# Kernel tuning notes

Measured on AMD Instinct MI355X. Metric: run time of the kernel, lower is better.

## Reference

```python
import jax, jax.numpy as jnp
import numpy as np

D_K = 64
SCALE = 1.0 / (D_K ** 0.5)
NEG = -1.0e9

def setup_inputs() -> dict:
    key = jax.random.key(0)
    kq, kk, kv, km = jax.random.split(key, 4)
    B, H, S, D = 4, 16, 2048, D_K
    query = jax.random.normal(kq, (B, H, S, D), dtype=jnp.float32)
    k_ = jax.random.normal(kk, (B, H, S, D), dtype=jnp.float32)
    v_ = jax.random.normal(kv, (B, H, S, D), dtype=jnp.float32)
    mask = jax.random.randint(km, (B, 1, S, S), 0, 2, dtype=jnp.int32)
    return {"query": query, "key": k_, "value": v_, "mask": mask}

def reference(query, key, value, mask):
    # scores: [B, H, S, S]
    scores = jnp.einsum('bhqd,bhkd->bhqk', query, key) * SCALE
    scores = jnp.where(mask == 0, NEG, scores)
    attn = jax.nn.softmax(scores, axis=-1)
    return jnp.einsum('bhqk,bhkd->bhqd', attn, value)
```

## Files before the change

kernel.cpp:

```cpp
#include <hip/hip_runtime.h>

typedef _Float16 f16x8 __attribute__((ext_vector_type(8)));
typedef _Float16 f16x4 __attribute__((ext_vector_type(4)));
typedef _Float16 f16x2 __attribute__((ext_vector_type(2)));
typedef float    f32x4 __attribute__((ext_vector_type(4)));
typedef unsigned long long u64;

constexpr int Bc = 4, Hc = 16, Sc = 2048, Dc = 64;
constexpr int KVBLK = 64;
constexpr int NKV = Sc / KVBLK;
constexpr int QB  = 128;
constexpr int NQT = Sc / QB;
constexpr int NQ  = 32;

__device__ __forceinline__ float fast_exp2(float x) {
#if __has_builtin(__builtin_amdgcn_exp2f)
  return __builtin_amdgcn_exp2f(x);
#else
  return exp2f(x);
#endif
}

__device__ __forceinline__ void gload16(const void* g, void* l) {
  __builtin_amdgcn_global_load_lds(
      (const __attribute__((address_space(1))) void*)g,
      (__attribute__((address_space(3))) void*)l, 16, 0, 0);
}

__device__ __forceinline__ f32x4 mfma16(f16x8 a, f16x8 b, f32x4 c) {
  return __builtin_amdgcn_mfma_f32_16x16x32_f16(a, b, c, 0, 0, 0);
}

__device__ __forceinline__ float dot2acc(unsigned pk, float acc) {
#if __has_builtin(__builtin_amdgcn_fdot2)
  const f16x2 one2 = {(_Float16)1.f, (_Float16)1.f};
  return __builtin_amdgcn_fdot2(__builtin_bit_cast(f16x2, pk), one2, acc, false);
#else
  const f16x2 v = __builtin_bit_cast(f16x2, pk);
  return acc + (float)v[0] + (float)v[1];
#endif
}

__global__ __launch_bounds__(256)
void cvt_k_sw(const float* __restrict__ K, _Float16* __restrict__ Ko) {
  const int tile = blockIdx.x;
  const int t = threadIdx.x;
  const float* src = K + (size_t)tile * 4096;
  _Float16* dst = Ko + (size_t)tile * 4096;
  #pragma unroll
  for (int cc = 0; cc < 2; ++cc) {
    const int c = t + cc * 256;
    const int r = c >> 3, s = c & 7;
    const int ss = s ^ (r & 7);
    const float* p = src + r * 64 + ss * 8;
    const float4 a = *(const float4*)p;
    const float4 b2 = *(const float4*)(p + 4);
    f16x8 h = {(_Float16)a.x, (_Float16)a.y, (_Float16)a.z, (_Float16)a.w,
               (_Float16)b2.x, (_Float16)b2.y, (_Float16)b2.z, (_Float16)b2.w};
    *(f16x8*)(dst + (size_t)c * 8) = h;
  }
}

__global__ __launch_bounds__(256)
void cvt_v_sw(const float* __restrict__ V, _Float16* __restrict__ Vo) {
  __shared__ float tile[64][65];
  const int tb = blockIdx.x;
  const int t = threadIdx.x;
  const float* src = V + (size_t)tb * 4096;
  {
    const int r = t >> 2, c0 = (t & 3) * 16;
    #pragma unroll
    for (int j = 0; j < 16; j += 4)
      *(float4*)&tile[r][c0 + j] = *(const float4*)(src + r * 64 + c0 + j);
  }
  __syncthreads();
  _Float16* dst = Vo + (size_t)tb * 4096;
  #pragma unroll
  for (int cc = 0; cc < 2; ++cc) {
    const int c = t + cc * 256;
    const int d = c >> 3, ss = c & 7;
    const int m = ss ^ (d & 7);
    const int ks = m >> 2, lg = m & 3;
    f16x8 h;
    #pragma unroll
    for (int e = 0; e < 8; ++e) {
      const int key = 32 * ks + 16 * (e >> 2) + 4 * lg + (e & 3);
      h[e] = (_Float16)tile[key][d];
    }
    *(f16x8*)(dst + (size_t)c * 8) = h;
  }
}

__global__ __launch_bounds__(256)
void pack_mask(const int* __restrict__ M, u64* __restrict__ MB) {
  const int gid  = blockIdx.x * 256 + threadIdx.x;
  const int wv   = gid >> 6, lane = gid & 63;
  const int kv   = wv & (NKV - 1);
  const int row  = (wv >> 5) & (Sc - 1);
  const int b    = wv >> 16;
  const int m    = M[((size_t)b * Sc + row) * Sc + (size_t)kv * 64 + lane];
  const u64 bits = __ballot(m != 0);
  if (lane == 0)
    MB[(((size_t)b * NQ + (row >> 6)) * NKV + kv) * 64 + (row & 63)] = bits;
}

__global__ __launch_bounds__(256, 4)
void attn_fwd6(const float* __restrict__ Q, const _Float16* __restrict__ Ksw,
               const _Float16* __restrict__ Vsw, const u64* __restrict__ MB,
               float* __restrict__ O)
{
  const int bid = (blockIdx.x & 7) * 128 + (blockIdx.x >> 3);
  const int qt  = bid & (NQT - 1);
  const int bh  = bid >> 4;
  const int b   = bh >> 4;
  const int q0  = qt * QB;

  const int tid = threadIdx.x;
  const int w   = tid >> 6;
  const int l   = tid & 63;
  const int lg  = l >> 4;
  const int lc  = l & 15;

  __shared__ _Float16 Kbuf0[4096], Kbuf1[4096];
  __shared__ _Float16 Vbuf0[4096], Vbuf1[4096];

  f16x8 qf[2][2];
  {
    const float qs = 0.125f * 1.4426950408889634f;
    #pragma unroll
    for (int qa = 0; qa < 2; ++qa) {
      const float* qr = Q + ((size_t)bh * Sc + q0 + w * 32 + qa * 16 + lc) * Dc + 8 * lg;
      #pragma unroll
      for (int ks = 0; ks < 2; ++ks) {
        f16x8 t;
        #pragma unroll
        for (int e = 0; e < 8; ++e) t[e] = (_Float16)(qr[ks * 32 + e] * qs);
        qf[qa][ks] = t;
      }
    }
  }

  f32x4 o_acc[2][4];
  #pragma unroll
  for (int qa = 0; qa < 2; ++qa)
    #pragma unroll
    for (int nt = 0; nt < 4; ++nt) o_acc[qa][nt] = (f32x4){0.f, 0.f, 0.f, 0.f};
  float l_acc0 = 0.f, l_acc1 = 0.f;
  const float NEGL = -1.4426950e9f;

  const char* KswT = (const char*)(Ksw + (size_t)bh * Sc * Dc);
  const char* VswT = (const char*)(Vsw + (size_t)bh * Sc * Dc);
  const int row0 = q0 + w * 32 + lc;
  const int row1 = row0 + 16;
  const u64* Mb0 = MB + ((size_t)(b * NQ + (row0 >> 6)) * NKV) * 64 + (row0 & 63);
  const u64* Mb1 = MB + ((size_t)(b * NQ + (row1 >> 6)) * NKV) * 64 + (row1 & 63);

  const int sw0 = (lg * 16) ^ ((lc & 7) << 4);
  const int sw1 = (64 + lg * 16) ^ ((lc & 7) << 4);

  auto stage = [&](int kvt, _Float16* kb, _Float16* vb) {
    const char* g = (w < 2) ? KswT + (size_t)kvt * 8192 + w * 4096
                            : VswT + (size_t)kvt * 8192 + (w - 2) * 4096;
    char* lb = (w < 2) ? (char*)kb + w * 4096
                       : (char*)vb + (w - 2) * 4096;
    #pragma unroll
    for (int j = 0; j < 4; ++j)
      gload16(g + j * 1024 + l * 16, lb + j * 1024);
  };

  auto body = [&](const _Float16* kb, const _Float16* vb, u64 mb0, u64 mb1) {
    const char* Kb = (const char*)kb;
    f32x4 p[2][4];
    __builtin_amdgcn_s_setprio(1);
    #pragma unroll
    for (int nt = 0; nt < 4; ++nt) {
      const f16x8 k0 = *(const f16x8*)(Kb + (nt * 16 + lc) * 128 + sw0);
      const f16x8 k1 = *(const f16x8*)(Kb + (nt * 16 + lc) * 128 + sw1);
      #pragma unroll
      for (int qa = 0; qa < 2; ++qa) {
        f32x4 acc = (f32x4){0.f, 0.f, 0.f, 0.f};
        acc = mfma16(k0, qf[qa][0], acc);
        acc = mfma16(k1, qf[qa][1], acc);
        p[qa][nt] = acc;
      }
    }
    __builtin_amdgcn_s_setprio(0);

    #pragma unroll
    for (int qa = 0; qa < 2; ++qa) {
      const u64 mbits = qa ? mb1 : mb0;
      #pragma unroll
      for (int nt = 0; nt < 4; ++nt) {
        const unsigned b4 = ((unsigned)(mbits >> (nt * 16 + 4 * lg))) & 0xFu;
        #pragma unroll
        for (int r = 0; r < 4; ++r) {
          const float s = ((b4 >> r) & 1u) ? p[qa][nt][r] : NEGL;
          p[qa][nt][r] = fast_exp2(s);
        }
      }
    }

    f16x8 pa0[2], pa1[2];
    #pragma unroll
    for (int qa = 0; qa < 2; ++qa) {
      uint4 u0, u1;
      u0.x = __builtin_bit_cast(unsigned, __builtin_amdgcn_cvt_pkrtz(p[qa][0][0], p[qa][0][1]));
      u0.y = __builtin_bit_cast(unsigned, __builtin_amdgcn_cvt_pkrtz(p[qa][0][2], p[qa][0][3]));
      u0.z = __builtin_bit_cast(unsigned, __builtin_amdgcn_cvt_pkrtz(p[qa][1][0], p[qa][1][1]));
      u0.w = __builtin_bit_cast(unsigned, __builtin_amdgcn_cvt_pkrtz(p[qa][1][2], p[qa][1][3]));
      u1.x = __builtin_bit_cast(unsigned, __builtin_amdgcn_cvt_pkrtz(p[qa][2][0], p[qa][2][1]));
      u1.y = __builtin_bit_cast(unsigned, __builtin_amdgcn_cvt_pkrtz(p[qa][2][2], p[qa][2][3]));
      u1.z = __builtin_bit_cast(unsigned, __builtin_amdgcn_cvt_pkrtz(p[qa][3][0], p[qa][3][1]));
      u1.w = __builtin_bit_cast(unsigned, __builtin_amdgcn_cvt_pkrtz(p[qa][3][2], p[qa][3][3]));
      float la = qa ? l_acc1 : l_acc0;
      la = dot2acc(u0.x, la); la = dot2acc(u0.y, la);
      la = dot2acc(u0.z, la); la = dot2acc(u0.w, la);
      la = dot2acc(u1.x, la); la = dot2acc(u1.y, la);
      la = dot2acc(u1.z, la); la = dot2acc(u1.w, la);
      if (qa) l_acc1 = la; else l_acc0 = la;
      pa0[qa] = __builtin_bit_cast(f16x8, u0);
      pa1[qa] = __builtin_bit_cast(f16x8, u1);
    }

    const char* Vb = (const char*)vb;
    __builtin_amdgcn_s_setprio(1);
    #pragma unroll
    for (int nt = 0; nt < 4; ++nt) {
      const f16x8 v0 = *(const f16x8*)(Vb + (nt * 16 + lc) * 128 + sw0);
      const f16x8 v1 = *(const f16x8*)(Vb + (nt * 16 + lc) * 128 + sw1);
      o_acc[0][nt] = mfma16(pa0[0], v0, o_acc[0][nt]);
      o_acc[0][nt] = mfma16(pa1[0], v1, o_acc[0][nt]);
      o_acc[1][nt] = mfma16(pa0[1], v0, o_acc[1][nt]);
      o_acc[1][nt] = mfma16(pa1[1], v1, o_acc[1][nt]);
    }
    __builtin_amdgcn_s_setprio(0);
  };

  u64 n0 = Mb0[0], n1 = Mb1[0];
  stage(0, Kbuf0, Vbuf0);
  __syncthreads();
  for (int kv = 0; kv < NKV; kv += 2) {
    const u64 a0 = n0, a1 = n1;
    const u64 c0 = Mb0[(size_t)(kv + 1) * 64];
    const u64 c1 = Mb1[(size_t)(kv + 1) * 64];
    stage(kv + 1, Kbuf1, Vbuf1);
    body(Kbuf0, Vbuf0, a0, a1);
    __syncthreads();
    if (kv + 2 < NKV) {
      n0 = Mb0[(size_t)(kv + 2) * 64];
      n1 = Mb1[(size_t)(kv + 2) * 64];
      stage(kv + 2, Kbuf0, Vbuf0);
    }
    body(Kbuf1, Vbuf1, c0, c1);
    __syncthreads();
  }

  l_acc0 += __shfl_xor(l_acc0, 16, 64);
  l_acc0 += __shfl_xor(l_acc0, 32, 64);
  l_acc1 += __shfl_xor(l_acc1, 16, 64);
  l_acc1 += __shfl_xor(l_acc1, 32, 64);
  #pragma unroll
  for (int qa = 0; qa < 2; ++qa) {
    #pragma unroll
    for (int r = 0; r < 4; ++r) {
      const float li = 1.0f / __shfl(qa ? l_acc1 : l_acc0, 4 * lg + r, 64);
      float* orow = O + ((size_t)bh * Sc + q0 + w * 32 + qa * 16 + 4 * lg + r) * Dc + lc;
      #pragma unroll
      for (int nt = 0; nt < 4; ++nt)
        orow[nt * 16] = o_acc[qa][nt][r] * li;
    }
  }
}

constexpr int LDSW = KVBLK + 8;

__global__ __launch_bounds__(256)
void attn_fwd_v1(const float* __restrict__ Q, const float* __restrict__ K,
                 const float* __restrict__ V, const int* __restrict__ M,
                 float* __restrict__ O)
{
  const int bid   = blockIdx.x;
  const int qtile = bid & 31;
  const int bh    = bid >> 5;
  const int b     = bh >> 4;

  const float* Qp = Q + ((size_t)bh * Sc + (size_t)qtile * 64) * Dc;
  const float* Kp = K + (size_t)bh * Sc * Dc;
  const float* Vp = V + (size_t)bh * Sc * Dc;
  const int*   Mp = M + (size_t)b * Sc * Sc + (size_t)qtile * 64 * Sc;
  float*       Op = O + ((size_t)bh * Sc + (size_t)qtile * 64) * Dc;

  __shared__ _Float16 Klds [KVBLK][LDSW];
  __shared__ _Float16 Vtlds[Dc]   [LDSW];
  __shared__ _Float16 Pl   [64]   [LDSW];

  const int tid = threadIdx.x;
  const int w   = tid >> 6;
  const int l   = tid & 63;
  const int lg  = l >> 4;
  const int lc  = l & 15;

  f16x8 qf[2];
  {
    const float qs = 0.125f * 1.4426950408889634f;
    const float* qrow = Qp + (size_t)(w * 16 + lc) * Dc + 8 * lg;
    #pragma unroll
    for (int ks = 0; ks < 2; ++ks) {
      f16x8 t;
      #pragma unroll
      for (int e = 0; e < 8; ++e) t[e] = (_Float16)(qrow[ks * 32 + e] * qs);
      qf[ks] = t;
    }
  }

  f32x4 o_acc[4];
  #pragma unroll
  for (int nt = 0; nt < 4; ++nt) o_acc[nt] = (f32x4){0.f, 0.f, 0.f, 0.f};
  float m_r[4], l_r[4];
  #pragma unroll
  for (int r = 0; r < 4; ++r) { m_r[r] = -3.0e38f; l_r[r] = 0.f; }
  const float NEGL = -1.4426950e9f;

  for (int kv = 0; kv < NKV; ++kv) {
    const float* Kt = Kp + (size_t)kv * KVBLK * Dc;
    const float* Vt = Vp + (size_t)kv * KVBLK * Dc;
    __syncthreads();
    {
      const int r = tid >> 2, c0 = (tid & 3) * 16;
      const float* src = Kt + (size_t)r * Dc + c0;
      f16x8 h0, h1;
      #pragma unroll
      for (int e = 0; e < 8; ++e) h0[e] = (_Float16)src[e];
      #pragma unroll
      for (int e = 0; e < 8; ++e) h1[e] = (_Float16)src[8 + e];
      *(f16x8*)&Klds[r][c0]     = h0;
      *(f16x8*)&Klds[r][c0 + 8] = h1;
    }
    {
      const int r0 = (tid >> 4) * 4, c0 = (tid & 15) * 4;
      float a_[4][4];
      #pragma unroll
      for (int i = 0; i < 4; ++i) {
        const float4 v4 = *(const float4*)(Vt + (size_t)(r0 + i) * Dc + c0);
        a_[i][0] = v4.x; a_[i][1] = v4.y; a_[i][2] = v4.z; a_[i][3] = v4.w;
      }
      #pragma unroll
      for (int j = 0; j < 4; ++j) {
        f16x4 t = {(_Float16)a_[0][j], (_Float16)a_[1][j],
                   (_Float16)a_[2][j], (_Float16)a_[3][j]};
        *(f16x4*)&Vtlds[c0 + j][r0] = t;
      }
    }
    __syncthreads();

    f32x4 s_acc[4];
    #pragma unroll
    for (int nt = 0; nt < 4; ++nt) {
      f32x4 acc = (f32x4){0.f, 0.f, 0.f, 0.f};
      #pragma unroll
      for (int ks = 0; ks < 2; ++ks) {
        f16x8 kf = *(const f16x8*)&Klds[nt * 16 + lc][ks * 32 + 8 * lg];
        acc = __builtin_amdgcn_mfma_f32_16x16x32_f16(qf[ks], kf, acc, 0, 0, 0);
      }
      s_acc[nt] = acc;
    }

    const int* mbase = Mp + (size_t)kv * KVBLK + lc;
    #pragma unroll
    for (int r = 0; r < 4; ++r) {
      const int qrow = w * 16 + 4 * lg + r;
      const int* mr = mbase + (size_t)qrow * Sc;
      float s0 = (mr[0]  != 0) ? s_acc[0][r] : NEGL;
      float s1 = (mr[16] != 0) ? s_acc[1][r] : NEGL;
      float s2 = (mr[32] != 0) ? s_acc[2][r] : NEGL;
      float s3 = (mr[48] != 0) ? s_acc[3][r] : NEGL;
      float mx = fmaxf(fmaxf(s0, s1), fmaxf(s2, s3));
      #pragma unroll
      for (int off = 1; off < 16; off <<= 1)
        mx = fmaxf(mx, __shfl_xor(mx, off, 64));
      const float mn   = fmaxf(m_r[r], mx);
      const float corr = fast_exp2(m_r[r] - mn);
      m_r[r] = mn;
      float p0 = fast_exp2(s0 - mn);
      float p1 = fast_exp2(s1 - mn);
      float p2 = fast_exp2(s2 - mn);
      float p3 = fast_exp2(s3 - mn);
      float rs = (p0 + p1) + (p2 + p3);
      #pragma unroll
      for (int off = 1; off < 16; off <<= 1)
        rs += __shfl_xor(rs, off, 64);
      l_r[r] = l_r[r] * corr + rs;
      #pragma unroll
      for (int nt = 0; nt < 4; ++nt) o_acc[nt][r] *= corr;
      Pl[qrow][lc]      = (_Float16)p0;
      Pl[qrow][16 + lc] = (_Float16)p1;
      Pl[qrow][32 + lc] = (_Float16)p2;
      Pl[qrow][48 + lc] = (_Float16)p3;
    }

    #pragma unroll
    for (int nt = 0; nt < 4; ++nt) {
      #pragma unroll
      for (int ks = 0; ks < 2; ++ks) {
        f16x8 pf = *(const f16x8*)&Pl[w * 16 + lc][ks * 32 + 8 * lg];
        f16x8 vf = *(const f16x8*)&Vtlds[nt * 16 + lc][ks * 32 + 8 * lg];
        o_acc[nt] = __builtin_amdgcn_mfma_f32_16x16x32_f16(pf, vf, o_acc[nt], 0, 0, 0);
      }
    }
  }

  #pragma unroll
  for (int r = 0; r < 4; ++r) {
    const float inv = 1.0f / l_r[r];
    float* orow = Op + (size_t)(w * 16 + 4 * lg + r) * Dc;
    #pragma unroll
    for (int nt = 0; nt < 4; ++nt)
      orow[nt * 16 + lc] = o_acc[nt][r] * inv;
  }
}

extern "C" void kernel_launch(void* const* d_in, const int* in_sizes, int n_in,
                              void* d_out, int out_size, void* d_ws, size_t ws_size,
                              hipStream_t stream) {
  (void)in_sizes; (void)n_in; (void)out_size;
  const float* Q = (const float*)d_in[0];
  const float* K = (const float*)d_in[1];
  const float* V = (const float*)d_in[2];
  const int*   M = (const int*)d_in[3];
  float*       O = (float*)d_out;

  const size_t nKV      = (size_t)Bc * Hc * Sc * Dc;
  const size_t bytesK16 = nKV * 2;
  const size_t bytesMB  = (size_t)Bc * NQ * NKV * 64 * 8;
  const size_t need     = 2 * bytesK16 + bytesMB;

  if (ws_size >= need) {
    _Float16* K16  = (_Float16*)d_ws;
    _Float16* Vt16 = (_Float16*)((char*)d_ws + bytesK16);
    u64*      MBp  = (u64*)((char*)d_ws + 2 * bytesK16);
    hipLaunchKernelGGL(cvt_k_sw,  dim3(2048),  dim3(256), 0, stream, K, K16);
    hipLaunchKernelGGL(cvt_v_sw,  dim3(2048),  dim3(256), 0, stream, V, Vt16);
    hipLaunchKernelGGL(pack_mask, dim3(65536), dim3(256), 0, stream, M, MBp);
    hipLaunchKernelGGL(attn_fwd6, dim3(1024),  dim3(256), 0, stream, Q, K16, Vt16, MBp, O);
  } else {
    hipLaunchKernelGGL(attn_fwd_v1, dim3(2048), dim3(256), 0, stream, Q, K, V, M, O);
  }
}
```

Measured before the change: 134.0 us.

## Double Q tile to 256 rows with 512-thread blocks and manual vmcnt pipelining

Raises the query tile per block from 128 to 256 rows by using 8 waves, so each staged K/V tile is shared by twice as many query rows and total K/V traffic is halved. The grid shrinks from 1024 to 512 blocks. Synchronisation now uses explicit s_waitcnt vmcnt plus raw s_barrier instead of __syncthreads, so the prefetch of the next tile can stay in flight while the current one is consumed. Fewer blocks may hurt load balance across CUs, and the hand-written waitcnt counts must match the number of outstanding loads to stay correct.

```diff
diff --git a/kernel.cpp b/kernel.cpp
--- a/kernel.cpp
+++ b/kernel.cpp
@@ -4,12 +4,13 @@
 typedef _Float16 f16x4 __attribute__((ext_vector_type(4)));
 typedef _Float16 f16x2 __attribute__((ext_vector_type(2)));
 typedef float    f32x4 __attribute__((ext_vector_type(4)));
+typedef unsigned u32x4 __attribute__((ext_vector_type(4)));
 typedef unsigned long long u64;
 
 constexpr int Bc = 4, Hc = 16, Sc = 2048, Dc = 64;
 constexpr int KVBLK = 64;
 constexpr int NKV = Sc / KVBLK;
-constexpr int QB  = 128;
+constexpr int QB  = 256;
 constexpr int NQT = Sc / QB;
 constexpr int NQ  = 32;
 
@@ -29,6 +30,10 @@
 
 __device__ __forceinline__ f32x4 mfma16(f16x8 a, f16x8 b, f32x4 c) {
   return __builtin_amdgcn_mfma_f32_16x16x32_f16(a, b, c, 0, 0, 0);
+}
+
+__device__ __forceinline__ unsigned pkrtz(float x, float y) {
+  return __builtin_bit_cast(unsigned, __builtin_amdgcn_cvt_pkrtz(x, y));
 }
 
 __device__ __forceinline__ float dot2acc(unsigned pk, float acc) {
@@ -104,14 +109,14 @@
     MB[(((size_t)b * NQ + (row >> 6)) * NKV + kv) * 64 + (row & 63)] = bits;
 }
 
-__global__ __launch_bounds__(256, 4)
-void attn_fwd6(const float* __restrict__ Q, const _Float16* __restrict__ Ksw,
-               const _Float16* __restrict__ Vsw, const u64* __restrict__ MB,
-               float* __restrict__ O)
+__global__ __launch_bounds__(512, 4)
+void attn_fwd11(const float* __restrict__ Q, const _Float16* __restrict__ Ksw,
+                const _Float16* __restrict__ Vsw, const u64* __restrict__ MB,
+                float* __restrict__ O)
 {
-  const int bid = (blockIdx.x & 7) * 128 + (blockIdx.x >> 3);
+  const int bid = (blockIdx.x & 7) * 64 + (blockIdx.x >> 3);
   const int qt  = bid & (NQT - 1);
-  const int bh  = bid >> 4;
+  const int bh  = bid >> 3;
   const int b   = bh >> 4;
   const int q0  = qt * QB;
 
@@ -121,8 +126,11 @@
   const int lg  = l >> 4;
   const int lc  = l & 15;
 
-  __shared__ _Float16 Kbuf0[4096], Kbuf1[4096];
-  __shared__ _Float16 Vbuf0[4096], Vbuf1[4096];
+  __shared__ _Float16 SB[16384];
+  const char* sb = (const char*)SB;
+
+  const int a0 = lc * 128 + (((0 + lg) ^ (lc & 7)) << 4);
+  const int a1 = lc * 128 + (((4 + lg) ^ (lc & 7)) << 4);
 
   f16x8 qf[2][2];
   {
@@ -155,27 +163,22 @@
   const u64* Mb0 = MB + ((size_t)(b * NQ + (row0 >> 6)) * NKV) * 64 + (row0 & 63);
   const u64* Mb1 = MB + ((size_t)(b * NQ + (row1 >> 6)) * NKV) * 64 + (row1 & 63);
 
-  const int sw0 = (lg * 16) ^ ((lc & 7) << 4);
-  const int sw1 = (64 + lg * 16) ^ ((lc & 7) << 4);
-
-  auto stage = [&](int kvt, _Float16* kb, _Float16* vb) {
-    const char* g = (w < 2) ? KswT + (size_t)kvt * 8192 + w * 4096
-                            : VswT + (size_t)kvt * 8192 + (w - 2) * 4096;
-    char* lb = (w < 2) ? (char*)kb + w * 4096
-                       : (char*)vb + (w - 2) * 4096;
-    #pragma unroll
-    for (int j = 0; j < 4; ++j)
-      gload16(g + j * 1024 + l * 16, lb + j * 1024);
+  auto stage = [&](int kvt, int buf) {
+    const char* g = (w < 4) ? KswT + (size_t)kvt * 8192 + w * 2048
+                            : VswT + (size_t)kvt * 8192 + (w - 4) * 2048;
+    char* lb = (char*)SB + buf * 16384 + ((w < 4) ? w * 2048 : 8192 + (w - 4) * 2048);
+    gload16(g + l * 16, lb);
+    gload16(g + 1024 + l * 16, lb + 1024);
   };
 
-  auto body = [&](const _Float16* kb, const _Float16* vb, u64 mb0, u64 mb1) {
-    const char* Kb = (const char*)kb;
+  auto body = [&](int buf, u64 m0, u64 m1) {
+    const int base = buf * 16384;
     f32x4 p[2][4];
     __builtin_amdgcn_s_setprio(1);
     #pragma unroll
     for (int nt = 0; nt < 4; ++nt) {
-      const f16x8 k0 = *(const f16x8*)(Kb + (nt * 16 + lc) * 128 + sw0);
-      const f16x8 k1 = *(const f16x8*)(Kb + (nt * 16 + lc) * 128 + sw1);
+      const f16x8 k0 = *(const f16x8*)(sb + base + nt * 2048 + a0);
+      const f16x8 k1 = *(const f16x8*)(sb + base + nt * 2048 + a1);
       #pragma unroll
       for (int qa = 0; qa < 2; ++qa) {
         f32x4 acc = (f32x4){0.f, 0.f, 0.f, 0.f};
@@ -185,49 +188,38 @@
       }
     }
     __builtin_amdgcn_s_setprio(0);
-
     #pragma unroll
     for (int qa = 0; qa < 2; ++qa) {
-      const u64 mbits = qa ? mb1 : mb0;
+      const u64 mbits = qa ? m1 : m0;
       #pragma unroll
       for (int nt = 0; nt < 4; ++nt) {
         const unsigned b4 = ((unsigned)(mbits >> (nt * 16 + 4 * lg))) & 0xFu;
         #pragma unroll
-        for (int r = 0; r < 4; ++r) {
-          const float s = ((b4 >> r) & 1u) ? p[qa][nt][r] : NEGL;
-          p[qa][nt][r] = fast_exp2(s);
-        }
-      }
-    }
-
+        for (int r = 0; r < 4; ++r)
+          p[qa][nt][r] = fast_exp2(((b4 >> r) & 1u) ? p[qa][nt][r] : NEGL);
+      }
+    }
     f16x8 pa0[2], pa1[2];
     #pragma unroll
     for (int qa = 0; qa < 2; ++qa) {
-      uint4 u0, u1;
-      u0.x = __builtin_bit_cast(unsigned, __builtin_amdgcn_cvt_pkrtz(p[qa][0][0], p[qa][0][1]));
-      u0.y = __builtin_bit_cast(unsigned, __builtin_amdgcn_cvt_pkrtz(p[qa][0][2], p[qa][0][3]));
-      u0.z = __builtin_bit_cast(unsigned, __builtin_amdgcn_cvt_pkrtz(p[qa][1][0], p[qa][1][1]));
-      u0.w = __builtin_bit_cast(unsigned, __builtin_amdgcn_cvt_pkrtz(p[qa][1][2], p[qa][1][3]));
-      u1.x = __builtin_bit_cast(unsigned, __builtin_amdgcn_cvt_pkrtz(p[qa][2][0], p[qa][2][1]));
-      u1.y = __builtin_bit_cast(unsigned, __builtin_amdgcn_cvt_pkrtz(p[qa][2][2], p[qa][2][3]));
-      u1.z = __builtin_bit_cast(unsigned, __builtin_amdgcn_cvt_pkrtz(p[qa][3][0], p[qa][3][1]));
-      u1.w = __builtin_bit_cast(unsigned, __builtin_amdgcn_cvt_pkrtz(p[qa][3][2], p[qa][3][3]));
+      u32x4 u0, u1;
+      #pragma unroll
+      for (int i = 0; i < 4; ++i) {
+        u0[i] = pkrtz(p[qa][i >> 1][(i & 1) * 2], p[qa][i >> 1][(i & 1) * 2 + 1]);
+        u1[i] = pkrtz(p[qa][2 + (i >> 1)][(i & 1) * 2], p[qa][2 + (i >> 1)][(i & 1) * 2 + 1]);
+      }
       float la = qa ? l_acc1 : l_acc0;
-      la = dot2acc(u0.x, la); la = dot2acc(u0.y, la);
-      la = dot2acc(u0.z, la); la = dot2acc(u0.w, la);
-      la = dot2acc(u1.x, la); la = dot2acc(u1.y, la);
-      la = dot2acc(u1.z, la); la = dot2acc(u1.w, la);
+      #pragma unroll
+      for (int i = 0; i < 4; ++i) { la = dot2acc(u0[i], la); la = dot2acc(u1[i], la); }
       if (qa) l_acc1 = la; else l_acc0 = la;
       pa0[qa] = __builtin_bit_cast(f16x8, u0);
       pa1[qa] = __builtin_bit_cast(f16x8, u1);
     }
-
-    const char* Vb = (const char*)vb;
     __builtin_amdgcn_s_setprio(1);
     #pragma unroll
     for (int nt = 0; nt < 4; ++nt) {
-      const f16x8 v0 = *(const f16x8*)(Vb + (nt * 16 + lc) * 128 + sw0);
-      const f16x8 v1 = *(const f16x8*)(Vb + (nt * 16 + lc) * 128 + sw1);
+      const f16x8 v0 = *(const f16x8*)(sb + base + 8192 + nt * 2048 + a0);
+      const f16x8 v1 = *(const f16x8*)(sb + base + 8192 + nt * 2048 + a1);
       o_acc[0][nt] = mfma16(pa0[0], v0, o_acc[0][nt]);
       o_acc[0][nt] = mfma16(pa1[0], v1, o_acc[0][nt]);
       o_acc[1][nt] = mfma16(pa0[1], v0, o_acc[1][nt]);
@@ -236,23 +228,35 @@
     __builtin_amdgcn_s_setprio(0);
   };
 
-  u64 n0 = Mb0[0], n1 = Mb1[0];
-  stage(0, Kbuf0, Vbuf0);
-  __syncthreads();
-  for (int kv = 0; kv < NKV; kv += 2) {
-    const u64 a0 = n0, a1 = n1;
-    const u64 c0 = Mb0[(size_t)(kv + 1) * 64];
-    const u64 c1 = Mb1[(size_t)(kv + 1) * 64];
-    stage(kv + 1, Kbuf1, Vbuf1);
-    body(Kbuf0, Vbuf0, a0, a1);
-    __syncthreads();
-    if (kv + 2 < NKV) {
-      n0 = Mb0[(size_t)(kv + 2) * 64];
-      n1 = Mb1[(size_t)(kv + 2) * 64];
-      stage(kv + 2, Kbuf0, Vbuf0);
-    }
-    body(Kbuf1, Vbuf1, c0, c1);
-    __syncthreads();
+  u64 mA0 = Mb0[0], mA1 = Mb1[0];
+  stage(0, 0);
+  asm volatile("s_waitcnt vmcnt(0)" ::: "memory");
+  __builtin_amdgcn_sched_barrier(0);
+  __builtin_amdgcn_s_barrier();
+
+  u64 mB0, mB1;
+  for (int t = 0; t < NKV; t += 2) {
+    stage(t + 1, 1);
+    mB0 = Mb0[(size_t)(t + 1) * 64];
+    mB1 = Mb1[(size_t)(t + 1) * 64];
+    asm volatile("s_waitcnt vmcnt(4)" ::: "memory");
+    __builtin_amdgcn_sched_barrier(0);
+    __builtin_amdgcn_s_barrier();
+    body(0, mA0, mA1);
+    __builtin_amdgcn_s_barrier();
+
+    if (t + 2 < NKV) {
+      stage(t + 2, 0);
+      mA0 = Mb0[(size_t)(t + 2) * 64];
+      mA1 = Mb1[(size_t)(t + 2) * 64];
+      asm volatile("s_waitcnt vmcnt(4)" ::: "memory");
+    } else {
+      asm volatile("s_waitcnt vmcnt(0)" ::: "memory");
+    }
+    __builtin_amdgcn_sched_barrier(0);
+    __builtin_amdgcn_s_barrier();
+    body(1, mB0, mB1);
+    __builtin_amdgcn_s_barrier();
   }
 
   l_acc0 += __shfl_xor(l_acc0, 16, 64);
@@ -438,10 +442,10 @@
     _Float16* K16  = (_Float16*)d_ws;
     _Float16* Vt16 = (_Float16*)((char*)d_ws + bytesK16);
     u64*      MBp  = (u64*)((char*)d_ws + 2 * bytesK16);
-    hipLaunchKernelGGL(cvt_k_sw,  dim3(2048),  dim3(256), 0, stream, K, K16);
-    hipLaunchKernelGGL(cvt_v_sw,  dim3(2048),  dim3(256), 0, stream, V, Vt16);
-    hipLaunchKernelGGL(pack_mask, dim3(65536), dim3(256), 0, stream, M, MBp);
-    hipLaunchKernelGGL(attn_fwd6, dim3(1024),  dim3(256), 0, stream, Q, K16, Vt16, MBp, O);
+    hipLaunchKernelGGL(cvt_k_sw,   dim3(2048),  dim3(256), 0, stream, K, K16);
+    hipLaunchKernelGGL(cvt_v_sw,   dim3(2048),  dim3(256), 0, stream, V, Vt16);
+    hipLaunchKernelGGL(pack_mask,  dim3(65536), dim3(256), 0, stream, M, MBp);
+    hipLaunchKernelGGL(attn_fwd11, dim3(512),   dim3(512), 0, stream, Q, K16, Vt16, MBp, O);
   } else {
     hipLaunchKernelGGL(attn_fwd_v1, dim3(2048), dim3(256), 0, stream, Q, K, V, M, O);
   }
```

After: 130.2 us (median of 3 runs). 1.03x faster.
